# Kernel tuning notes

Measured on AMD Instinct MI355X. Metric: run time of the kernel, lower is better.

The kernel has to match this reference:

```python
import jax, jax.numpy as jnp
import numpy as np

B, L, H2 = 64, 512, 1024  # batch, question length, 2*hidden_dim


def setup_inputs() -> dict:
    key = jax.random.key(0)
    ks = jax.random.split(key, 9)
    sc = 1.0 / np.sqrt(H2)
    return {
        "s_t_hat": jax.random.normal(ks[0], (B, H2), dtype=jnp.float32),
        "pai_q": jax.random.normal(ks[1], (B, L, H2), dtype=jnp.float32),
        "que_padding_mask": (jax.random.uniform(ks[2], (B, L)) > 0.1).astype(jnp.float32),
        "que_coverage": jax.random.uniform(ks[3], (B, L), dtype=jnp.float32),
        "W_q": jax.random.normal(ks[4], (H2, H2), dtype=jnp.float32) * sc,
        "W_qs_w": jax.random.normal(ks[5], (H2, H2), dtype=jnp.float32) * sc,
        "W_qs_b": jax.random.normal(ks[6], (H2,), dtype=jnp.float32) * sc,
        "W_c": jax.random.normal(ks[7], (1, H2), dtype=jnp.float32) * sc,
        "v_q": jax.random.normal(ks[8], (H2, 1), dtype=jnp.float32) * sc,
    }


def reference(s_t_hat, pai_q, que_padding_mask, que_coverage, W_q, W_qs_w, W_qs_b, W_c, v_q):
    # encoder feature: (b, l, 2h)
    enc_feat = jnp.einsum("blh,hk->blk", pai_q, W_q)
    # decoder feature: (b, 2h) -> broadcast over l
    dec_feat = s_t_hat @ W_qs_w + W_qs_b
    att = enc_feat + dec_feat[:, None, :]
    # coverage feature: (b, l, 1) @ (1, 2h)
    att = att + que_coverage[:, :, None] * W_c[0][None, None, :]
    e = jnp.tanh(att)                                  # (b, l, 2h)
    scores = jnp.einsum("blh,ho->bl", e, v_q)          # (b, l)
    alpha = jax.nn.softmax(scores, axis=1) * que_padding_mask
    alpha = alpha / jnp.sum(alpha, axis=1, keepdims=True)
    c_q_t = jnp.einsum("bl,blh->bh", alpha, pai_q)      # (b, 2h)
    new_cov = que_coverage + alpha
    return (c_q_t, alpha, new_cov)
```

## Files before the change

### kernel.cpp

```cpp
#include <hip/hip_runtime.h>
#include <hip/hip_bf16.h>

#define B_   64
#define L_   512
#define H2_  1024
#define M_   (B_ * L_)
#define KSPLIT 16
#define KCH  (H2_ / KSPLIT)

typedef short bf16x8 __attribute__((ext_vector_type(8)));
typedef float f32x4  __attribute__((ext_vector_type(4)));
typedef ushort ushort8_t __attribute__((ext_vector_type(8)));

__device__ __forceinline__ ushort f2bf(float f) {
    uint x = __float_as_uint(f);
    uint r = (x + 0x7FFFu + ((x >> 16) & 1u)) >> 16;
    return (ushort)r;
}

__device__ __forceinline__ void gload_lds16(const ushort* g, ushort* l) {
    __builtin_amdgcn_global_load_lds(
        (const __attribute__((address_space(1))) void*)g,
        (__attribute__((address_space(3))) void*)l, 16, 0, 0);
}

__global__ __launch_bounds__(256) void convertA_kernel(
    const float* __restrict__ in, ushort* __restrict__ out)
{
    size_t i = ((size_t)blockIdx.x * 256 + threadIdx.x) * 8;
    float4 a = *(const float4*)&in[i];
    float4 b = *(const float4*)&in[i + 4];
    ushort8_t h;
    h[0] = f2bf(a.x); h[1] = f2bf(a.y); h[2] = f2bf(a.z); h[3] = f2bf(a.w);
    h[4] = f2bf(b.x); h[5] = f2bf(b.y); h[6] = f2bf(b.z); h[7] = f2bf(b.w);
    *(ushort8_t*)&out[i] = h;
}

__global__ __launch_bounds__(256) void convertB_kernel(
    const float* __restrict__ W, ushort* __restrict__ out)
{
    __shared__ float t[32][33];
    int tx = threadIdx.x & 31, ty = threadIdx.x >> 5;
    int k0 = blockIdx.x * 32, n0 = blockIdx.y * 32;
    #pragma unroll
    for (int r = 0; r < 4; ++r)
        t[ty + r * 8][tx] = W[(size_t)(k0 + ty + r * 8) * H2_ + n0 + tx];
    __syncthreads();
    #pragma unroll
    for (int r = 0; r < 4; ++r)
        out[(size_t)(n0 + ty + r * 8) * H2_ + k0 + tx] = f2bf(t[tx][ty + r * 8]);
}

__global__ __launch_bounds__(256) void dec_split_kernel(
    const float* __restrict__ s_t_hat, const float* __restrict__ Wqs,
    float* __restrict__ dec_part)
{
    const int t  = threadIdx.x;
    const int n  = blockIdx.x * 64 + (t & 63);
    const int k0 = blockIdx.y * KCH;
    const int bg = t >> 6;

    float acc[16];
    #pragma unroll
    for (int i = 0; i < 16; ++i) acc[i] = 0.f;

    for (int k8 = 0; k8 < KCH; k8 += 8) {
        float w[8];
        #pragma unroll
        for (int kk = 0; kk < 8; ++kk)
            w[kk] = Wqs[(size_t)(k0 + k8 + kk) * H2_ + n];
        #pragma unroll
        for (int i = 0; i < 16; ++i) {
            const float* srow = &s_t_hat[(bg * 16 + i) * H2_ + k0 + k8];
            #pragma unroll
            for (int kk = 0; kk < 8; ++kk)
                acc[i] += srow[kk] * w[kk];
        }
    }
    #pragma unroll
    for (int i = 0; i < 16; ++i)
        dec_part[(size_t)blockIdx.y * (B_ * H2_) + (bg * 16 + i) * H2_ + n] = acc[i];
}

__global__ __launch_bounds__(256) void dec_reduce_kernel(
    const float* __restrict__ dec_part, const float* __restrict__ bqs,
    float* __restrict__ dec)
{
    int i = blockIdx.x * 256 + threadIdx.x;
    float s = bqs[i & (H2_ - 1)];
    #pragma unroll
    for (int p = 0; p < KSPLIT; ++p) s += dec_part[(size_t)p * (B_ * H2_) + i];
    dec[i] = s;
}

__global__ __launch_bounds__(256) void dec_kernel(
    const float* __restrict__ s_t_hat, const float* __restrict__ Wqs,
    const float* __restrict__ bqs, float* __restrict__ dec)
{
    int n  = blockIdx.x * 256 + threadIdx.x;
    int b0 = blockIdx.y * 4;
    float a0 = 0.f, a1 = 0.f, a2 = 0.f, a3 = 0.f;
    for (int h = 0; h < H2_; ++h) {
        float w = Wqs[h * H2_ + n];
        a0 += s_t_hat[(b0 + 0) * H2_ + h] * w;
        a1 += s_t_hat[(b0 + 1) * H2_ + h] * w;
        a2 += s_t_hat[(b0 + 2) * H2_ + h] * w;
        a3 += s_t_hat[(b0 + 3) * H2_ + h] * w;
    }
    float bias = bqs[n];
    dec[(b0 + 0) * H2_ + n] = a0 + bias;
    dec[(b0 + 1) * H2_ + n] = a1 + bias;
    dec[(b0 + 2) * H2_ + n] = a2 + bias;
    dec[(b0 + 3) * H2_ + n] = a3 + bias;
}

#define BM 128
#define BN 128
#define BK 32

__global__ __launch_bounds__(256) void score_kernel2(
    const ushort* __restrict__ Abf,
    const ushort* __restrict__ Bbf,
    const float* __restrict__ dec,
    const float* __restrict__ cov,
    const float* __restrict__ Wc,
    const float* __restrict__ vq,
    float* __restrict__ scores_part)
{
    __shared__ ushort As[BM * BK];
    __shared__ ushort Bs[BN * BK];

    const int tid  = threadIdx.x;
    const int lane = tid & 63;
    const int wave = tid >> 6;
    const int wm = wave >> 1, wn = wave & 1;
    const int m0 = blockIdx.x * BM;
    const int n0 = blockIdx.y * BN;

    f32x4 acc[4][4] = {};

    const size_t arow = (size_t)(m0 + wave * 32 + (lane >> 2)) * H2_ + (lane & 3) * 8;
    const size_t brow = (size_t)(n0 + wave * 32 + (lane >> 2)) * H2_ + (lane & 3) * 8;
    ushort* lA0 = As + wave * 32 * BK;
    ushort* lA1 = lA0 + 16 * BK;
    ushort* lB0 = Bs + wave * 32 * BK;
    ushort* lB1 = lB0 + 16 * BK;

    const int fr = lane & 15;
    const int fg = lane >> 4;

    for (int kt = 0; kt < H2_; kt += BK) {
        gload_lds16(Abf + arow + kt, lA0);
        gload_lds16(Abf + arow + 16 * H2_ + kt, lA1);
        gload_lds16(Bbf + brow + kt, lB0);
        gload_lds16(Bbf + brow + 16 * H2_ + kt, lB1);
        __syncthreads();

        bf16x8 af[4], bfr[4];
        #pragma unroll
        for (int i = 0; i < 4; ++i)
            af[i] = *(const bf16x8*)&As[(wm * 64 + i * 16 + fr) * BK + fg * 8];
        #pragma unroll
        for (int j = 0; j < 4; ++j)
            bfr[j] = *(const bf16x8*)&Bs[(wn * 64 + j * 16 + fr) * BK + fg * 8];

        #pragma unroll
        for (int i = 0; i < 4; ++i)
            #pragma unroll
            for (int j = 0; j < 4; ++j)
                acc[i][j] = __builtin_amdgcn_mfma_f32_16x16x32_bf16(af[i], bfr[j], acc[i][j], 0, 0, 0);
        __syncthreads();
    }

    const int b = m0 >> 9;
    float dec4[4], wc4[4], vq4[4];
    #pragma unroll
    for (int j = 0; j < 4; ++j) {
        int n = n0 + wn * 64 + j * 16 + fr;
        dec4[j] = dec[b * H2_ + n];
        wc4[j]  = Wc[n];
        vq4[j]  = vq[n];
    }
    #pragma unroll
    for (int i = 0; i < 4; ++i) {
        #pragma unroll
        for (int r = 0; r < 4; ++r) {
            int ml = wm * 64 + i * 16 + fg * 4 + r;
            int m  = m0 + ml;
            float cv = cov[b * L_ + (m & (L_ - 1))];
            float s = 0.f;
            #pragma unroll
            for (int j = 0; j < 4; ++j) {
                float att = acc[i][j][r] + dec4[j] + cv * wc4[j];
                s += tanhf(att) * vq4[j];
            }
            s += __shfl_xor(s, 1);
            s += __shfl_xor(s, 2);
            s += __shfl_xor(s, 4);
            s += __shfl_xor(s, 8);
            if (fr == 0)
                scores_part[(size_t)(blockIdx.y * 2 + wn) * M_ + m] = s;
        }
    }
}

#define LDK 40
__global__ __launch_bounds__(256) void score_kernel_fb(
    const float* __restrict__ A, const float* __restrict__ Bmat,
    const float* __restrict__ dec, const float* __restrict__ cov,
    const float* __restrict__ Wc, const float* __restrict__ vq,
    float* __restrict__ scores_part)
{
    __shared__ ushort As[BM * LDK];
    __shared__ ushort Bs[BN * LDK];
    const int tid  = threadIdx.x;
    const int lane = tid & 63;
    const int wave = tid >> 6;
    const int wm = wave >> 1, wn = wave & 1;
    const int m0 = blockIdx.x * BM;
    const int n0 = blockIdx.y * BN;
    f32x4 acc[4][4] = {};
    const int a_row = tid >> 3;
    const int a_kc  = (tid & 7) * 4;
    const int b_k  = tid >> 5;
    const int b_nc = (tid & 31) * 4;
    const int fr = lane & 15;
    const int fg = lane >> 4;
    for (int kt = 0; kt < H2_; kt += BK) {
        #pragma unroll
        for (int p = 0; p < 4; ++p) {
            int row = a_row + p * 32;
            float4 v = *(const float4*)&A[(size_t)(m0 + row) * H2_ + kt + a_kc];
            ushort4 h;
            h.x = f2bf(v.x); h.y = f2bf(v.y); h.z = f2bf(v.z); h.w = f2bf(v.w);
            *(ushort4*)&As[row * LDK + a_kc] = h;
        }
        #pragma unroll
        for (int p = 0; p < 4; ++p) {
            int k = b_k + p * 8;
            float4 v = *(const float4*)&Bmat[(size_t)(kt + k) * H2_ + n0 + b_nc];
            Bs[(b_nc + 0) * LDK + k] = f2bf(v.x);
            Bs[(b_nc + 1) * LDK + k] = f2bf(v.y);
            Bs[(b_nc + 2) * LDK + k] = f2bf(v.z);
            Bs[(b_nc + 3) * LDK + k] = f2bf(v.w);
        }
        __syncthreads();
        bf16x8 af[4], bfr[4];
        #pragma unroll
        for (int i = 0; i < 4; ++i)
            af[i] = *(const bf16x8*)&As[(wm * 64 + i * 16 + fr) * LDK + fg * 8];
        #pragma unroll
        for (int j = 0; j < 4; ++j)
            bfr[j] = *(const bf16x8*)&Bs[(wn * 64 + j * 16 + fr) * LDK + fg * 8];
        #pragma unroll
        for (int i = 0; i < 4; ++i)
            #pragma unroll
            for (int j = 0; j < 4; ++j)
                acc[i][j] = __builtin_amdgcn_mfma_f32_16x16x32_bf16(af[i], bfr[j], acc[i][j], 0, 0, 0);
        __syncthreads();
    }
    const int b = m0 >> 9;
    float dec4[4], wc4[4], vq4[4];
    #pragma unroll
    for (int j = 0; j < 4; ++j) {
        int n = n0 + wn * 64 + j * 16 + fr;
        dec4[j] = dec[b * H2_ + n];
        wc4[j]  = Wc[n];
        vq4[j]  = vq[n];
    }
    #pragma unroll
    for (int i = 0; i < 4; ++i) {
        #pragma unroll
        for (int r = 0; r < 4; ++r) {
            int ml = wm * 64 + i * 16 + fg * 4 + r;
            int m  = m0 + ml;
            float cv = cov[b * L_ + (m & (L_ - 1))];
            float s = 0.f;
            #pragma unroll
            for (int j = 0; j < 4; ++j) {
                float att = acc[i][j][r] + dec4[j] + cv * wc4[j];
                s += tanhf(att) * vq4[j];
            }
            s += __shfl_xor(s, 1);
            s += __shfl_xor(s, 2);
            s += __shfl_xor(s, 4);
            s += __shfl_xor(s, 8);
            if (fr == 0)
                scores_part[(size_t)(blockIdx.y * 2 + wn) * M_ + m] = s;
        }
    }
}

__global__ __launch_bounds__(512) void softmax_kernel(
    const float* __restrict__ scores_part,
    const float* __restrict__ mask,
    const float* __restrict__ cov,
    float* __restrict__ out_alpha,
    float* __restrict__ out_newcov)
{
    int b = blockIdx.x;
    int l = threadIdx.x;
    int m = b * L_ + l;
    float s = 0.f;
    #pragma unroll
    for (int p = 0; p < 16; ++p) s += scores_part[(size_t)p * M_ + m];
    __shared__ float red[8];
    float mx = s;
    #pragma unroll
    for (int o = 1; o < 64; o <<= 1) mx = fmaxf(mx, __shfl_xor(mx, o));
    int wid = l >> 6;
    if ((l & 63) == 0) red[wid] = mx;
    __syncthreads();
    mx = red[0];
    #pragma unroll
    for (int p = 1; p < 8; ++p) mx = fmaxf(mx, red[p]);
    __syncthreads();
    float e = expf(s - mx) * mask[m];
    float sm = e;
    #pragma unroll
    for (int o = 1; o < 64; o <<= 1) sm += __shfl_xor(sm, o);
    if ((l & 63) == 0) red[wid] = sm;
    __syncthreads();
    float tot = 0.f;
    #pragma unroll
    for (int p = 0; p < 8; ++p) tot += red[p];
    float alpha = e / tot;
    out_alpha[m]  = alpha;
    out_newcov[m] = cov[m] + alpha;
}

__global__ __launch_bounds__(256) void cqt_bf_kernel(
    const float* __restrict__ alpha, const ushort* __restrict__ Abf,
    float* __restrict__ out)
{
    int b = blockIdx.y;
    int k = blockIdx.x * 256 + threadIdx.x;
    __shared__ float al[L_];
    al[threadIdx.x]       = alpha[b * L_ + threadIdx.x];
    al[threadIdx.x + 256] = alpha[b * L_ + threadIdx.x + 256];
    __syncthreads();
    float acc = 0.f;
    const ushort* p = &Abf[(size_t)b * L_ * H2_ + k];
    #pragma unroll 8
    for (int l = 0; l < L_; ++l) {
        float v = __uint_as_float((uint)p[(size_t)l * H2_] << 16);
        acc += al[l] * v;
    }
    out[b * H2_ + k] = acc;
}

__global__ __launch_bounds__(256) void cqt_kernel(
    const float* __restrict__ alpha, const float* __restrict__ pai_q,
    float* __restrict__ out)
{
    int b = blockIdx.y;
    int k = blockIdx.x * 256 + threadIdx.x;
    __shared__ float al[L_];
    al[threadIdx.x]       = alpha[b * L_ + threadIdx.x];
    al[threadIdx.x + 256] = alpha[b * L_ + threadIdx.x + 256];
    __syncthreads();
    float acc = 0.f;
    const float* p = &pai_q[(size_t)b * L_ * H2_ + k];
    #pragma unroll 8
    for (int l = 0; l < L_; ++l) acc += al[l] * p[(size_t)l * H2_];
    out[b * H2_ + k] = acc;
}

extern "C" void kernel_launch(void* const* d_in, const int* in_sizes, int n_in,
                              void* d_out, int out_size, void* d_ws, size_t ws_size,
                              hipStream_t stream)
{
    const float* s_t_hat = (const float*)d_in[0];
    const float* pai_q   = (const float*)d_in[1];
    const float* mask    = (const float*)d_in[2];
    const float* cov     = (const float*)d_in[3];
    const float* W_q     = (const float*)d_in[4];
    const float* W_qs_w  = (const float*)d_in[5];
    const float* W_qs_b  = (const float*)d_in[6];
    const float* W_c     = (const float*)d_in[7];
    const float* v_q     = (const float*)d_in[8];

    float* out     = (float*)d_out;
    float* c_q_t   = out;
    float* alpha   = out + B_ * H2_;
    float* newcov  = alpha + B_ * L_;

    char* ws = (char*)d_ws;
    float*  dec         = (float*)ws;
    float*  scores_part = (float*)(ws + 262144);
    ushort* Bbf         = (ushort*)(ws + 262144 + 2097152);
    ushort* Abf         = (ushort*)(ws + 262144 + 2097152 + 2097152);
    float*  dec_part    = (float*)Abf;
    const size_t ws_needed = 262144ull + 2097152ull + 2097152ull + 67108864ull;

    if (ws_size >= ws_needed) {
        dec_split_kernel<<<dim3(16, KSPLIT), 256, 0, stream>>>(s_t_hat, W_qs_w, dec_part);
        dec_reduce_kernel<<<dim3(B_ * H2_ / 256), 256, 0, stream>>>(dec_part, W_qs_b, dec);
        convertA_kernel<<<dim3((M_ * H2_) / (256 * 8)), 256, 0, stream>>>(pai_q, Abf);
        convertB_kernel<<<dim3(32, 32), 256, 0, stream>>>(W_q, Bbf);
        score_kernel2<<<dim3(M_ / BM, H2_ / BN), 256, 0, stream>>>(
            Abf, Bbf, dec, cov, W_c, v_q, scores_part);
        softmax_kernel<<<dim3(B_), 512, 0, stream>>>(scores_part, mask, cov, alpha, newcov);
        cqt_bf_kernel<<<dim3(4, B_), 256, 0, stream>>>(alpha, Abf, c_q_t);
    } else {
        dec_kernel<<<dim3(4, 16), 256, 0, stream>>>(s_t_hat, W_qs_w, W_qs_b, dec);
        score_kernel_fb<<<dim3(M_ / BM, H2_ / BN), 256, 0, stream>>>(
            pai_q, W_q, dec, cov, W_c, v_q, scores_part);
        softmax_kernel<<<dim3(B_), 512, 0, stream>>>(scores_part, mask, cov, alpha, newcov);
        cqt_kernel<<<dim3(4, B_), 256, 0, stream>>>(alpha, pai_q, c_q_t);
    }
}
```

Baseline: 192.8 us.

## Double GEMM K-tile with XOR-swizzled LDS layout and use fast tanh

Raises the score GEMM K-tile from 32 to 64 and stores A/B tiles in LDS with an XOR swizzle on 16-byte column groups, so fragment reads avoid bank conflicts and the loop runs half as many barrier-separated iterations. Each B fragment is now reused across the i loop inside the MFMA loop. It also swaps tanhf for an exp-based fast_tanh in the epilogue of both score kernels, which trades some accuracy for fewer instructions. The fallback kernel keeps a fixed step of 32 so it is unaffected by the BK change.

```diff
diff --git a/kernel.cpp b/kernel.cpp
--- a/kernel.cpp
+++ b/kernel.cpp
@@ -16,6 +16,13 @@
     uint x = __float_as_uint(f);
     uint r = (x + 0x7FFFu + ((x >> 16) & 1u)) >> 16;
     return (ushort)r;
+}
+
+__device__ __forceinline__ float fast_tanh(float x) {
+    float ax = fabsf(x);
+    float e  = __expf(-2.0f * ax);
+    float t  = 1.0f - 2.0f * e / (1.0f + e);
+    return copysignf(t, x);
 }
 
 __device__ __forceinline__ void gload_lds16(const ushort* g, ushort* l) {
@@ -116,9 +123,9 @@
 
 #define BM 128
 #define BN 128
-#define BK 32
-
-__global__ __launch_bounds__(256) void score_kernel2(
+#define BK 64
+
+__global__ __launch_bounds__(256) void score_kernel3(
     const ushort* __restrict__ Abf,
     const ushort* __restrict__ Bbf,
     const float* __restrict__ dec,
@@ -139,36 +146,45 @@
 
     f32x4 acc[4][4] = {};
 
-    const size_t arow = (size_t)(m0 + wave * 32 + (lane >> 2)) * H2_ + (lane & 3) * 8;
-    const size_t brow = (size_t)(n0 + wave * 32 + (lane >> 2)) * H2_ + (lane & 3) * 8;
-    ushort* lA0 = As + wave * 32 * BK;
-    ushort* lA1 = lA0 + 16 * BK;
-    ushort* lB0 = Bs + wave * 32 * BK;
-    ushort* lB1 = lB0 + 16 * BK;
+    const int srow = lane >> 3;
+    const int scol = ((lane & 7) ^ srow) * 8;
+    const size_t abase = (size_t)(m0 + wave * 32 + srow) * H2_ + scol;
+    const size_t bbase = (size_t)(n0 + wave * 32 + srow) * H2_ + scol;
+    ushort* lA = As + wave * 32 * BK;
+    ushort* lB = Bs + wave * 32 * BK;
 
     const int fr = lane & 15;
     const int fg = lane >> 4;
+    const int fx = fr & 7;
 
     for (int kt = 0; kt < H2_; kt += BK) {
-        gload_lds16(Abf + arow + kt, lA0);
-        gload_lds16(Abf + arow + 16 * H2_ + kt, lA1);
-        gload_lds16(Bbf + brow + kt, lB0);
-        gload_lds16(Bbf + brow + 16 * H2_ + kt, lB1);
+        #pragma unroll
+        for (int p = 0; p < 4; ++p) {
+            gload_lds16(Abf + abase + p * 8 * H2_ + kt, lA + p * 8 * BK);
+            gload_lds16(Bbf + bbase + p * 8 * H2_ + kt, lB + p * 8 * BK);
+        }
         __syncthreads();
 
-        bf16x8 af[4], bfr[4];
+        bf16x8 af[4][2];
         #pragma unroll
         for (int i = 0; i < 4; ++i)
-            af[i] = *(const bf16x8*)&As[(wm * 64 + i * 16 + fr) * BK + fg * 8];
-        #pragma unroll
-        for (int j = 0; j < 4; ++j)
-            bfr[j] = *(const bf16x8*)&Bs[(wn * 64 + j * 16 + fr) * BK + fg * 8];
-
-        #pragma unroll
-        for (int i = 0; i < 4; ++i)
-            #pragma unroll
-            for (int j = 0; j < 4; ++j)
-                acc[i][j] = __builtin_amdgcn_mfma_f32_16x16x32_bf16(af[i], bfr[j], acc[i][j], 0, 0, 0);
+            #pragma unroll
+            for (int ks = 0; ks < 2; ++ks)
+                af[i][ks] = *(const bf16x8*)
+                    &As[(wm * 64 + i * 16 + fr) * BK + (((fg + ks * 4) ^ fx) * 8)];
+
+        #pragma unroll
+        for (int j = 0; j < 4; ++j) {
+            bf16x8 b0 = *(const bf16x8*)
+                &Bs[(wn * 64 + j * 16 + fr) * BK + ((fg ^ fx) * 8)];
+            bf16x8 b1 = *(const bf16x8*)
+                &Bs[(wn * 64 + j * 16 + fr) * BK + (((fg + 4) ^ fx) * 8)];
+            #pragma unroll
+            for (int i = 0; i < 4; ++i) {
+                acc[i][j] = __builtin_amdgcn_mfma_f32_16x16x32_bf16(af[i][0], b0, acc[i][j], 0, 0, 0);
+                acc[i][j] = __builtin_amdgcn_mfma_f32_16x16x32_bf16(af[i][1], b1, acc[i][j], 0, 0, 0);
+            }
+        }
         __syncthreads();
     }
 
@@ -192,7 +208,7 @@
             #pragma unroll
             for (int j = 0; j < 4; ++j) {
                 float att = acc[i][j][r] + dec4[j] + cv * wc4[j];
-                s += tanhf(att) * vq4[j];
+                s += fast_tanh(att) * vq4[j];
             }
             s += __shfl_xor(s, 1);
             s += __shfl_xor(s, 2);
@@ -226,7 +242,7 @@
     const int b_nc = (tid & 31) * 4;
     const int fr = lane & 15;
     const int fg = lane >> 4;
-    for (int kt = 0; kt < H2_; kt += BK) {
+    for (int kt = 0; kt < H2_; kt += 32) {
         #pragma unroll
         for (int p = 0; p < 4; ++p) {
             int row = a_row + p * 32;
@@ -279,7 +295,7 @@
             #pragma unroll
             for (int j = 0; j < 4; ++j) {
                 float att = acc[i][j][r] + dec4[j] + cv * wc4[j];
-                s += tanhf(att) * vq4[j];
+                s += fast_tanh(att) * vq4[j];
             }
             s += __shfl_xor(s, 1);
             s += __shfl_xor(s, 2);
@@ -398,7 +414,7 @@
         dec_reduce_kernel<<<dim3(B_ * H2_ / 256), 256, 0, stream>>>(dec_part, W_qs_b, dec);
         convertA_kernel<<<dim3((M_ * H2_) / (256 * 8)), 256, 0, stream>>>(pai_q, Abf);
         convertB_kernel<<<dim3(32, 32), 256, 0, stream>>>(W_q, Bbf);
-        score_kernel2<<<dim3(M_ / BM, H2_ / BN), 256, 0, stream>>>(
+        score_kernel3<<<dim3(M_ / BM, H2_ / BN), 256, 0, stream>>>(
             Abf, Bbf, dec, cov, W_c, v_q, scores_part);
         softmax_kernel<<<dim3(B_), 512, 0, stream>>>(scores_part, mask, cov, alpha, newcov);
         cqt_bf_kernel<<<dim3(4, B_), 256, 0, stream>>>(alpha, Abf, c_q_t);
```

After: 186.4 us. 3.3% less time.
